# Performance work log

Measured on AMD Instinct MI355X. Metric: run time of the kernel, lower is better.

## Reference

```python
import jax, jax.numpy as jnp
import numpy as np

B, T, D = 2, 2048, 2048
N, K, H = 16, 8, 128            # heads, kv heads, head_dim
SOFT_CAP = 50.0
WINDOW = 1024
SCALE = H ** -0.5               # query_pre_attn_scalar
ROPE_BASE = 10000.0
ROPE_SCALE = 1.0
K_MASK = -2.3819763e+38


def rms_norm(x, scale, eps=1e-6):
    var = jnp.mean(jnp.square(x), axis=-1, keepdims=True)
    return x * jax.lax.rsqrt(var + eps) * (1.0 + scale)


def apply_rope(x, positions):
    # x: [B,T,heads,H]; positions: [B,T] int
    head_dim = x.shape[-1]
    fraction = 2.0 * jnp.arange(head_dim // 2, dtype=jnp.float32) / head_dim
    timescale = ROPE_BASE ** fraction                      # [H/2]
    sinusoid = positions[..., None].astype(jnp.float32) / timescale  # [B,T,H/2]
    sinusoid = sinusoid[..., None, :] / ROPE_SCALE          # [B,T,1,H/2]
    sin, cos = jnp.sin(sinusoid), jnp.cos(sinusoid)
    first, second = jnp.split(x, 2, axis=-1)
    return jnp.concatenate([first * cos - second * sin,
                            second * cos + first * sin], axis=-1)


def setup_inputs() -> dict:
    key = jax.random.key(0)
    ks = jax.random.split(key, 6)
    x = jax.random.normal(ks[0], (B, T, D), jnp.float32)
    q_w = jax.random.normal(ks[1], (N, D, H), jnp.float32) * (D ** -0.5)
    kv_w = jax.random.normal(ks[2], (2, K, D, H), jnp.float32) * (D ** -0.5)
    o_w = jax.random.normal(ks[3], (N, H, D), jnp.float32) * ((N * H) ** -0.5)
    qnorm_scale = 0.1 * jax.random.normal(ks[4], (H,), jnp.float32)
    knorm_scale = 0.1 * jax.random.normal(ks[5], (H,), jnp.float32)
    segment_pos = jnp.broadcast_to(jnp.arange(T, dtype=jnp.int32), (B, T))
    attn_mask = jnp.broadcast_to(jnp.tril(jnp.ones((T, T), dtype=bool)), (B, T, T))
    return {"x": x, "q_w": q_w, "kv_w": kv_w, "o_w": o_w,
            "qnorm_scale": qnorm_scale, "knorm_scale": knorm_scale,
            "segment_pos": segment_pos, "attn_mask": attn_mask}


def reference(x, q_w, kv_w, o_w, qnorm_scale, knorm_scale, segment_pos, attn_mask):
    # projections
    q = jnp.einsum('BTD,NDH->BTNH', x, q_w)            # [B,T,N,H]
    k = jnp.einsum('BSD,KDH->BSKH', x, kv_w[0])        # [B,T,K,H]
    v = jnp.einsum('BSD,KDH->BSKH', x, kv_w[1])
    # QK RMSNorm, then RoPE, then query scaling (matches source order)
    q = apply_rope(rms_norm(q, qnorm_scale), segment_pos) * SCALE
    k = apply_rope(rms_norm(k, knorm_scale), segment_pos)
    # GQA: regroup query heads per kv head
    G = N // K
    qg = q.reshape(B, T, K, G, H)
    logits = jnp.einsum('BTKGH,BSKH->BTKGS', qg, k).reshape(B, T, N, T)
    # logit soft cap
    logits = jnp.tanh(logits / SOFT_CAP) * SOFT_CAP
    # sliding window mask combined with causal attn_mask
    pos_q = segment_pos[:, :, None]
    pos_k = segment_pos[:, None, :]
    sliding = (pos_k > pos_q - WINDOW) & (pos_k < pos_q + WINDOW)
    mask = attn_mask & sliding                          # [B,T,S]
    padded = jnp.where(mask[:, :, None, :], logits, K_MASK)
    probs = jax.nn.softmax(padded, axis=-1).astype(k.dtype)
    enc = jnp.einsum('BTKGS,BSKH->BTKGH',
                     probs.reshape(B, T, K, G, T), v).reshape(B, T, N, H)
    return jnp.einsum('BTNH,NHD->BTD', enc, o_w)
```

## Files before the change

kernel.cpp:

```cpp
#include <hip/hip_runtime.h>
#include <stdint.h>

#define BB 2
#define TT 2048
#define DD 2048
#define NHD 16
#define KVH 8
#define HD 128
#define JC 4096
#define WIN 1024
#define SCALE_Q 0.08838834764831845f

typedef __attribute__((ext_vector_type(8))) short bf16x8;
typedef __attribute__((ext_vector_type(8))) unsigned short us8;
typedef __attribute__((ext_vector_type(4))) unsigned short us4;
typedef __attribute__((ext_vector_type(4))) float f32x4;
typedef __attribute__((ext_vector_type(16))) float f32x16;
typedef __attribute__((ext_vector_type(4))) unsigned int u32x4;

#define GAS __attribute__((address_space(1)))
#define LAS __attribute__((address_space(3)))

__device__ __forceinline__ unsigned short f2bf(float f) {
  unsigned u = __float_as_uint(f);
  u += 0x7FFFu + ((u >> 16) & 1u);
  return (unsigned short)(u >> 16);
}
__device__ __forceinline__ float bf2f(unsigned short u) {
  return __uint_as_float(((unsigned)u) << 16);
}

__device__ __forceinline__ void gload16(const void* g, void* l) {
  __builtin_amdgcn_global_load_lds((const GAS unsigned int*)g, (LAS unsigned int*)l, 16, 0, 0);
}

#define VMCNT(n) asm volatile("s_waitcnt vmcnt(" #n ")" ::: "memory")

__global__ void __launch_bounds__(256) k_cvt(const float4* __restrict__ in,
                                             us4* __restrict__ out, int n4) {
  int i = blockIdx.x * 256 + threadIdx.x;
  if (i >= n4) return;
  float4 v = in[i];
  us4 o;
  o[0] = f2bf(v.x); o[1] = f2bf(v.y); o[2] = f2bf(v.z); o[3] = f2bf(v.w);
  out[i] = o;
}

__global__ void __launch_bounds__(256) k_transpose_cvt(
    const float* __restrict__ in, unsigned short* __restrict__ out,
    int R, int C, int ldin, long b0s, int nbi, long b1s, long obs) {
  __shared__ float tile[32][33];
  int z = blockIdx.z;
  const float* ib = in + (long)(z / nbi) * b0s + (long)(z % nbi) * b1s;
  unsigned short* ob = out + (long)z * obs;
  int c0 = blockIdx.x * 32, r0 = blockIdx.y * 32;
  int tx = threadIdx.x, ty = threadIdx.y;
#pragma unroll
  for (int i = 0; i < 4; i++)
    tile[ty + i * 8][tx] = ib[(long)(r0 + ty + i * 8) * ldin + c0 + tx];
  __syncthreads();
#pragma unroll
  for (int i = 0; i < 4; i++)
    ob[(long)(c0 + ty + i * 8) * R + r0 + tx] = f2bf(tile[tx][ty + i * 8]);
}

__global__ void __launch_bounds__(256) k_wt(const float* __restrict__ qw,
                                            const float* __restrict__ kvw,
                                            unsigned short* __restrict__ out) {
  __shared__ float tile[32][33];
  int z = blockIdx.z;
  const float* ib = (z < 16) ? qw + (long)z * 2048 * 128 : kvw + (long)(z - 16) * 2048 * 128;
  unsigned short* ob = out + (long)z * 128 * 2048;
  int c0 = blockIdx.x * 32, r0 = blockIdx.y * 32;
  int tx = threadIdx.x, ty = threadIdx.y;
#pragma unroll
  for (int i = 0; i < 4; i++)
    tile[ty + i * 8][tx] = ib[(long)(r0 + ty + i * 8) * 128 + c0 + tx];
  __syncthreads();
#pragma unroll
  for (int i = 0; i < 4; i++)
    ob[(long)(c0 + ty + i * 8) * 2048 + r0 + tx] = f2bf(tile[tx][ty + i * 8]);
}

__global__ void __launch_bounds__(256) k_transpose_bf(
    const unsigned short* __restrict__ in, unsigned short* __restrict__ out,
    int R, int C, int ldin, long b0s, int nbi, long b1s, long obs) {
  __shared__ unsigned short tile[32][33];
  int z = blockIdx.z;
  const unsigned short* ib = in + (long)(z / nbi) * b0s + (long)(z % nbi) * b1s;
  unsigned short* ob = out + (long)z * obs;
  int c0 = blockIdx.x * 32, r0 = blockIdx.y * 32;
  int tx = threadIdx.x, ty = threadIdx.y;
#pragma unroll
  for (int i = 0; i < 4; i++)
    tile[ty + i * 8][tx] = ib[(long)(r0 + ty + i * 8) * ldin + c0 + tx];
  __syncthreads();
#pragma unroll
  for (int i = 0; i < 4; i++)
    ob[(long)(c0 + ty + i * 8) * R + r0 + tx] = tile[tx][ty + i * 8];
}

template <int BM, int BN, int NWN, int THREADS, int NBUF, bool BF16OUT>
__global__ void __launch_bounds__(THREADS, 2) k_gemm9(
    const unsigned short* __restrict__ A, const unsigned short* __restrict__ Bt,
    void* __restrict__ Cv, int M, int Nn, int nby) {
  constexpr int KD = 2048;
  constexpr int NT = KD / 32;
  constexpr int ROWS = BM + BN;
  constexpr int RPI = THREADS / 4;
  constexpr int IA = BM / RPI;
  constexpr int IPT = ROWS / RPI;
  constexpr int MT = 8, MT2 = 4;
  __shared__ short lds[NBUF][ROWS * 32];

  int tid = threadIdx.x, lane = tid & 63, w = tid >> 6;
  int wm = w / NWN, wn = w % NWN;
  int id = blockIdx.x;
  int cpx = gridDim.x >> 3;
  id = (id & 7) * cpx + (id >> 3);
  int m0 = (id / nby) * BM, n0 = (id % nby) * BN;

  int srow = tid >> 2;
  int scol = ((tid & 3) ^ ((tid >> 3) & 3)) * 8;
  const unsigned short* gA = A + (long)(m0 + srow) * KD + scol;
  const unsigned short* gB = Bt + (long)(n0 + srow) * KD + scol;

  auto STG = [&](int p, int ko, int j) {
    if (j < IA)
      gload16(gA + (long)j * RPI * KD + ko, &lds[p][(j * RPI + w * 16) * 32]);
    else
      gload16(gB + (long)(j - IA) * RPI * KD + ko,
              &lds[p][(BM + (j - IA) * RPI + w * 16) * 32]);
  };

  int frag = (lane & 15) * 32 + (((lane >> 4) ^ ((lane >> 1) & 3)) * 8);
  int abase = wm * 128 * 32 + frag;
  int bbase = (BM + wn * 64) * 32 + frag;

  f32x4 acc[MT][4] = {};
#pragma unroll
  for (int tt = 0; tt < NBUF - 1; ++tt)
#pragma unroll
    for (int j = 0; j < IPT; ++j) STG(tt, tt * 32, j);
  if constexpr (IPT * (NBUF - 2) == 8) VMCNT(8);
  else VMCNT(6);
  __builtin_amdgcn_s_barrier();

  int buf = 0, sp = NBUF - 1;
  for (int t = 0; t < NT; ++t) {
    const short* bufp = lds[buf];
    bool st = (t + NBUF - 1) < NT;
    int ko = (t + NBUF - 1) * 32;
    bf16x8 bfr[4], af[MT2];
#pragma unroll
    for (int ni = 0; ni < 4; ++ni)
      bfr[ni] = *(const bf16x8*)&bufp[bbase + ni * 16 * 32];
#pragma unroll
    for (int mi = 0; mi < MT2; ++mi)
      af[mi] = *(const bf16x8*)&bufp[abase + mi * 16 * 32];
    if (st) {
#pragma unroll
      for (int j = 0; j < IPT / 2; ++j) STG(sp, ko, j);
    }
    __builtin_amdgcn_s_barrier();
    asm volatile("s_waitcnt lgkmcnt(0)" ::: "memory");
    __builtin_amdgcn_sched_barrier(0);
    __builtin_amdgcn_s_setprio(1);
#pragma unroll
    for (int mi = 0; mi < MT2; ++mi)
#pragma unroll
      for (int ni = 0; ni < 4; ++ni)
        acc[mi][ni] = __builtin_amdgcn_mfma_f32_16x16x32_bf16(af[mi], bfr[ni], acc[mi][ni], 0, 0, 0);
    __builtin_amdgcn_s_setprio(0);
    __builtin_amdgcn_s_barrier();
    bf16x8 af2[MT2];
#pragma unroll
    for (int mi = 0; mi < MT2; ++mi)
      af2[mi] = *(const bf16x8*)&bufp[abase + (MT2 + mi) * 16 * 32];
    if (st) {
#pragma unroll
      for (int j = IPT / 2; j < IPT; ++j) STG(sp, ko, j);
    }
    {
      int rem = NT - 2 - t;
      if (rem > NBUF - 2) rem = NBUF - 2;
      if (rem == 2) {
        if constexpr (IPT == 4) VMCNT(8); else VMCNT(12);
      } else if (rem == 1) {
        if constexpr (IPT == 4) VMCNT(4); else VMCNT(6);
      } else if (rem == 0) {
        VMCNT(0);
      }
    }
    __builtin_amdgcn_s_barrier();
    asm volatile("s_waitcnt lgkmcnt(0)" ::: "memory");
    __builtin_amdgcn_sched_barrier(0);
    __builtin_amdgcn_s_setprio(1);
#pragma unroll
    for (int mi = 0; mi < MT2; ++mi)
#pragma unroll
      for (int ni = 0; ni < 4; ++ni)
        acc[MT2 + mi][ni] = __builtin_amdgcn_mfma_f32_16x16x32_bf16(af2[mi], bfr[ni], acc[MT2 + mi][ni], 0, 0, 0);
    __builtin_amdgcn_s_setprio(0);
    __builtin_amdgcn_s_barrier();
    buf = (buf == NBUF - 1) ? 0 : buf + 1;
    sp = (sp == NBUF - 1) ? 0 : sp + 1;
  }

#pragma unroll
  for (int mi = 0; mi < MT; mi++)
#pragma unroll
    for (int ni = 0; ni < 4; ni++)
#pragma unroll
      for (int r = 0; r < 4; r++) {
        int row = m0 + wm * 128 + mi * 16 + (lane >> 4) * 4 + r;
        int col = n0 + wn * 64 + ni * 16 + (lane & 15);
        if constexpr (BF16OUT)
          ((unsigned short*)Cv)[(long)row * Nn + col] = f2bf(acc[mi][ni][r]);
        else
          ((float*)Cv)[(long)row * Nn + col] = acc[mi][ni][r];
      }
}

__global__ void __launch_bounds__(256) k_norm_rope(
    const unsigned short* __restrict__ qkv, const float* __restrict__ qns,
    const float* __restrict__ kns,
    unsigned short* __restrict__ qb, unsigned short* __restrict__ kb) {
  int wid = threadIdx.x >> 6, lane = threadIdx.x & 63;
  long r = (long)blockIdx.x * 4 + wid;
  int b = (int)(r / (TT * 24));
  int rem = (int)(r % (TT * 24));
  int t = rem / 24, hd = rem % 24;
  const unsigned short* row = qkv + (long)(b * TT + t) * JC + (hd < 16 ? hd * HD : 2048 + (hd - 16) * HD);
  float f0 = bf2f(row[lane]), f1 = bf2f(row[lane + 64]);
  float ss = f0 * f0 + f1 * f1;
#pragma unroll
  for (int m = 1; m < 64; m <<= 1) ss += __shfl_xor(ss, m, 64);
  float rinv = rsqrtf(ss * (1.0f / 128.0f) + 1e-6f);
  const float* sc = (hd < 16) ? qns : kns;
  float y0 = f0 * rinv * (1.0f + sc[lane]);
  float y1 = f1 * rinv * (1.0f + sc[lane + 64]);
  float ts = exp2f((float)lane * (13.287712379549449f / 64.0f));
  float ang = (float)t / ts;
  float s, c;
  sincosf(ang, &s, &c);
  float o0 = y0 * c - y1 * s;
  float o1 = y1 * c + y0 * s;
  unsigned short* dst;
  if (hd < 16) {
    o0 *= SCALE_Q; o1 *= SCALE_Q;
    dst = qb + ((long)(b * NHD + hd) * TT + t) * HD;
  } else {
    dst = kb + ((long)(b * KVH + (hd - 16)) * TT + t) * HD;
  }
  dst[lane] = f2bf(o0);
  dst[lane + 64] = f2bf(o1);
}

template <bool FULL>
__device__ __forceinline__ void softcap16(const f32x16& s16, float* pr, float& lsum,
                                          int s_base, int tq, int g) {
#pragma unroll
  for (int r = 0; r < 16; r++) {
    float x = s16[r];
    float e = __builtin_amdgcn_exp2f(-0.05770780163555853f * fabsf(x));
    float u = (x > 0.0f ? e : 1.0f) * __builtin_amdgcn_rcpf(1.0f + e);
    float p = __builtin_amdgcn_exp2f(-144.26950408889634f * u);
    if (!FULL) {
      int s = s_base + (r & 3) + 8 * (r >> 2) + 4 * g;
      bool valid = (s <= tq) && (s > tq - WIN);
      p = valid ? p : 0.0f;
    }
    lsum += p;
    pr[r] = p;
  }
}

__device__ __forceinline__ void hswap(unsigned& a, unsigned& b, int g) {
  unsigned ax = (unsigned)__shfl_xor((int)a, 32, 64);
  unsigned bx = (unsigned)__shfl_xor((int)b, 32, 64);
  unsigned r0 = g ? bx : a;
  unsigned r1 = g ? b : ax;
  a = r0; b = r1;
}

__global__ void __launch_bounds__(256, 1) k_attn(
    const unsigned short* __restrict__ qb, const unsigned short* __restrict__ kb,
    const unsigned short* __restrict__ vbT, unsigned short* __restrict__ enc) {
  __shared__ short Kl[2][64][128];
  __shared__ short Vt[2][128][64];
  int tid = threadIdx.x, lane = tid & 63, w = tid >> 6;
  int g = lane >> 5, l31 = lane & 31;
  int id = blockIdx.x;
  int b = id >> 7;
  int rem = id & 127;
  int n = rem >> 3;
  int ti = rem & 7;
  int t0 = ti * 256;
  int kh = n >> 1;
  const unsigned short* qbase = qb + ((long)(b * NHD + n) * TT + t0 + w * 64) * HD;
  const unsigned short* kbase = kb + (long)(b * KVH + kh) * TT * HD;
  const unsigned short* vbase = vbT + (long)(b * KVH + kh) * HD * TT;

  bf16x8 bq[2][8];
#pragma unroll
  for (int qg = 0; qg < 2; qg++) {
    const unsigned short* qp = qbase + (long)(qg * 32 + l31) * HD + g * 8;
#pragma unroll
    for (int kb8 = 0; kb8 < 8; kb8++)
      bq[qg][kb8] = *(const bf16x8*)(qp + kb8 * 16);
  }

  f32x16 acc0[4] = {}, acc1[4] = {};
  float lsum0 = 0.0f, lsum1 = 0.0f;
  int t0w = t0 + w * 64;
  int s_begin = (t0 >= WIN) ? t0 - WIN : 0;
  int s_end = t0 + 256;

  auto STAGE = [&](int buf, int s0) {
#pragma unroll
    for (int i = 0; i < 4; i++) {
      int row = w * 16 + i * 4 + (lane >> 4);
      int c16 = (lane & 15) ^ (row & 7);
      gload16(kbase + (long)(s0 + row) * HD + c16 * 8, &Kl[buf][w * 16 + i * 4][0]);
    }
#pragma unroll
    for (int i = 0; i < 4; i++) {
      int row = w * 32 + i * 8 + (lane >> 3);
      int c16 = (lane & 7) ^ (row & 7);
      gload16(vbase + (long)row * TT + s0 + c16 * 8, &Vt[buf][w * 32 + i * 8][0]);
    }
  };

  auto PROC = [&](const f32x16& sv, int qg, float& ls, unsigned (*pwp)[4], int sb, int s0) {
    int base = t0w + qg * 32;
    int tq = base + l31;
    float pr[16];
    bool fullg = (s0 + 63 <= base) && (s0 >= base + 32 - WIN);
    if (fullg) softcap16<true>(sv, pr, ls, 0, tq, g);
    else       softcap16<false>(sv, pr, ls, s0 + sb * 32, tq, g);
    unsigned X[4], Y[4];
#pragma unroll
    for (int m = 0; m < 4; m++) {
      asm("v_cvt_pk_bf16_f32 %0, %1, %2" : "=v"(X[m]) : "v"(pr[4 * m]), "v"(pr[4 * m + 1]));
      asm("v_cvt_pk_bf16_f32 %0, %1, %2" : "=v"(Y[m]) : "v"(pr[4 * m + 2]), "v"(pr[4 * m + 3]));
    }
#pragma unroll
    for (int kl = 0; kl < 2; kl++) {
      hswap(X[2 * kl], X[2 * kl + 1], g);
      hswap(Y[2 * kl], Y[2 * kl + 1], g);
      pwp[sb * 2 + kl][0] = X[2 * kl];
      pwp[sb * 2 + kl][1] = Y[2 * kl];
      pwp[sb * 2 + kl][2] = X[2 * kl + 1];
      pwp[sb * 2 + kl][3] = Y[2 * kl + 1];
    }
  };

  STAGE(0, s_begin);
  __syncthreads();
  int cur = 0;
  for (int s0 = s_begin; s0 < s_end; s0 += 64) {
    if (s0 + 64 < s_end) STAGE(cur ^ 1, s0 + 64);
    bool live = (s0 <= t0w + 63) && (s0 + 63 >= t0w - (WIN - 1));
    if (live) {
      unsigned pw0[4][4], pw1[4][4];
#pragma unroll
      for (int sb = 0; sb < 2; sb++) {
        int srow = sb * 32 + l31;
        f32x16 s0v = {}, s1v = {};
#pragma unroll
        for (int kb8 = 0; kb8 < 8; kb8++) {
          bf16x8 ak = *(const bf16x8*)&Kl[cur][srow][8 * ((2 * kb8 + g) ^ (srow & 7))];
          s0v = __builtin_amdgcn_mfma_f32_32x32x16_bf16(ak, bq[0][kb8], s0v, 0, 0, 0);
          s1v = __builtin_amdgcn_mfma_f32_32x32x16_bf16(ak, bq[1][kb8], s1v, 0, 0, 0);
        }
        PROC(s0v, 0, lsum0, pw0, sb, s0);
        PROC(s1v, 1, lsum1, pw1, sb, s0);
      }
#pragma unroll
      for (int ks = 0; ks < 4; ks++) {
        u32x4 t40 = {pw0[ks][0], pw0[ks][1], pw0[ks][2], pw0[ks][3]};
        u32x4 t41 = {pw1[ks][0], pw1[ks][1], pw1[ks][2], pw1[ks][3]};
        bf16x8 pb0 = __builtin_bit_cast(bf16x8, t40);
        bf16x8 pb1 = __builtin_bit_cast(bf16x8, t41);
#pragma unroll
        for (int ht = 0; ht < 4; ht++) {
          int hrow = ht * 32 + l31;
          bf16x8 av = *(const bf16x8*)&Vt[cur][hrow][8 * ((2 * ks + g) ^ (hrow & 7))];
          acc0[ht] = __builtin_amdgcn_mfma_f32_32x32x16_bf16(av, pb0, acc0[ht], 0, 0, 0);
          acc1[ht] = __builtin_amdgcn_mfma_f32_32x32x16_bf16(av, pb1, acc1[ht], 0, 0, 0);
        }
      }
    }
    __syncthreads();
    cur ^= 1;
  }

  lsum0 += __shfl_xor(lsum0, 32, 64);
  lsum1 += __shfl_xor(lsum1, 32, 64);
  float inv0 = __builtin_amdgcn_rcpf(lsum0);
  float inv1 = __builtin_amdgcn_rcpf(lsum1);
  unsigned short* dst0 = enc + ((long)(b * TT + t0w + l31) * NHD + n) * HD;
  unsigned short* dst1 = enc + ((long)(b * TT + t0w + 32 + l31) * NHD + n) * HD;
#pragma unroll
  for (int ht = 0; ht < 4; ht++)
#pragma unroll
    for (int r4 = 0; r4 < 4; r4++) {
      us4 o0, o1;
#pragma unroll
      for (int e = 0; e < 4; e++) {
        o0[e] = f2bf(acc0[ht][r4 * 4 + e] * inv0);
        o1[e] = f2bf(acc1[ht][r4 * 4 + e] * inv1);
      }
      *(us4*)(dst0 + ht * 32 + 8 * r4 + 4 * g) = o0;
      *(us4*)(dst1 + ht * 32 + 8 * r4 + 4 * g) = o1;
    }
}

extern "C" void kernel_launch(void* const* d_in, const int* in_sizes, int n_in,
                              void* d_out, int out_size, void* d_ws, size_t ws_size,
                              hipStream_t stream) {
  const float* x    = (const float*)d_in[0];
  const float* q_w  = (const float*)d_in[1];
  const float* kv_w = (const float*)d_in[2];
  const float* o_w  = (const float*)d_in[3];
  const float* qns  = (const float*)d_in[4];
  const float* kns  = (const float*)d_in[5];

  if (ws_size < (104ull << 20)) return;
  char* ws = (char*)d_ws;
  unsigned short* qkvb = (unsigned short*)(ws + 0);
  unsigned short* enc  = (unsigned short*)(ws + 0);
  unsigned short* x_bf = (unsigned short*)(ws + (64ll << 20));
  unsigned short* qb   = (unsigned short*)(ws + (64ll << 20));
  unsigned short* Wt   = (unsigned short*)(ws + (80ll << 20));
  unsigned short* kb   = (unsigned short*)(ws + (80ll << 20));
  unsigned short* vbT  = (unsigned short*)(ws + (88ll << 20));
  unsigned short* Wt_o = (unsigned short*)(ws + (96ll << 20));

  dim3 tb(32, 8, 1);
  k_cvt<<<8192, 256, 0, stream>>>((const float4*)x, (us4*)x_bf, 2097152);
  k_wt<<<dim3(4, 64, 32), tb, 0, stream>>>(q_w, kv_w, Wt);
  k_transpose_cvt<<<dim3(64, 64, 1), tb, 0, stream>>>(o_w, Wt_o, 2048, 2048, 2048, 0, 1, 0, 0);
  k_gemm9<256, 256, 4, 512, 4, true><<<256, 512, 0, stream>>>(x_bf, Wt, qkvb, 4096, 4096, 16);
  k_transpose_bf<<<dim3(4, 64, 16), tb, 0, stream>>>(qkvb + 3072, vbT, 2048, 128, 4096,
                                                     (long)2048 * 4096, 8, 128, (long)128 * 2048);
  k_norm_rope<<<24576, 256, 0, stream>>>(qkvb, qns, kns, qb, kb);
  k_attn<<<256, 256, 0, stream>>>(qb, kb, vbT, enc);
  k_gemm9<256, 128, 2, 256, 3, false><<<256, 256, 0, stream>>>(enc, Wt_o, (float*)d_out, 4096, 2048, 16);
}
```

Measured before the change: 250.5 us.

## Merge prep kernels, retile QKV GEMM and attention, simplify softcap

Merges the three input-conversion and transpose kernels into one launch, and the V transpose with norm/rope into another, cutting launch count. The QKV GEMM now uses 256x128 tiles with 512 blocks instead of 256x256 with 256 blocks. Attention uses 128-thread blocks of 128 queries with two blocks per CU and interleaves the tile order between batches for load balance. The softcap exponential loses its sign-split form, saving ALU ops but risking overflow in exp2 for large logits (rcp of inf gives 0, which still works).

```diff
diff --git a/kernel.cpp b/kernel.cpp
--- a/kernel.cpp
+++ b/kernel.cpp
@@ -36,68 +36,45 @@
 
 #define VMCNT(n) asm volatile("s_waitcnt vmcnt(" #n ")" ::: "memory")
 
-__global__ void __launch_bounds__(256) k_cvt(const float4* __restrict__ in,
-                                             us4* __restrict__ out, int n4) {
-  int i = blockIdx.x * 256 + threadIdx.x;
-  if (i >= n4) return;
-  float4 v = in[i];
-  us4 o;
-  o[0] = f2bf(v.x); o[1] = f2bf(v.y); o[2] = f2bf(v.z); o[3] = f2bf(v.w);
-  out[i] = o;
-}
-
-__global__ void __launch_bounds__(256) k_transpose_cvt(
-    const float* __restrict__ in, unsigned short* __restrict__ out,
-    int R, int C, int ldin, long b0s, int nbi, long b1s, long obs) {
+__global__ void __launch_bounds__(256) k_pre(
+    const float4* __restrict__ x4, us4* __restrict__ xb,
+    const float* __restrict__ qw, const float* __restrict__ kvw,
+    const float* __restrict__ ow, unsigned short* __restrict__ Wt,
+    unsigned short* __restrict__ Wt_o) {
   __shared__ float tile[32][33];
-  int z = blockIdx.z;
-  const float* ib = in + (long)(z / nbi) * b0s + (long)(z % nbi) * b1s;
-  unsigned short* ob = out + (long)z * obs;
-  int c0 = blockIdx.x * 32, r0 = blockIdx.y * 32;
-  int tx = threadIdx.x, ty = threadIdx.y;
+  int id = blockIdx.x;
+  int tid = threadIdx.x;
+  if (id < 8192) {
+    int i = id * 256 + tid;
+    float4 v = x4[i];
+    us4 o;
+    o[0] = f2bf(v.x); o[1] = f2bf(v.y); o[2] = f2bf(v.z); o[3] = f2bf(v.w);
+    xb[i] = o;
+    return;
+  }
+  const float* ib;
+  unsigned short* ob;
+  int ldin, c0, r0;
+  int t = id - 8192;
+  if (t < 8192) {
+    int bx = t & 3, by = (t >> 2) & 63, z = t >> 8;
+    ib = (z < 16) ? qw + (long)z * 2048 * 128 : kvw + (long)(z - 16) * 2048 * 128;
+    ob = Wt + (long)z * 128 * 2048;
+    ldin = 128;
+    c0 = bx * 32; r0 = by * 32;
+  } else {
+    int u = t - 8192;
+    ib = ow; ob = Wt_o; ldin = 2048;
+    c0 = (u & 63) * 32; r0 = (u >> 6) * 32;
+  }
+  int tx = tid & 31, ty = tid >> 5;
 #pragma unroll
   for (int i = 0; i < 4; i++)
     tile[ty + i * 8][tx] = ib[(long)(r0 + ty + i * 8) * ldin + c0 + tx];
   __syncthreads();
 #pragma unroll
   for (int i = 0; i < 4; i++)
-    ob[(long)(c0 + ty + i * 8) * R + r0 + tx] = f2bf(tile[tx][ty + i * 8]);
-}
-
-__global__ void __launch_bounds__(256) k_wt(const float* __restrict__ qw,
-                                            const float* __restrict__ kvw,
-                                            unsigned short* __restrict__ out) {
-  __shared__ float tile[32][33];
-  int z = blockIdx.z;
-  const float* ib = (z < 16) ? qw + (long)z * 2048 * 128 : kvw + (long)(z - 16) * 2048 * 128;
-  unsigned short* ob = out + (long)z * 128 * 2048;
-  int c0 = blockIdx.x * 32, r0 = blockIdx.y * 32;
-  int tx = threadIdx.x, ty = threadIdx.y;
-#pragma unroll
-  for (int i = 0; i < 4; i++)
-    tile[ty + i * 8][tx] = ib[(long)(r0 + ty + i * 8) * 128 + c0 + tx];
-  __syncthreads();
-#pragma unroll
-  for (int i = 0; i < 4; i++)
     ob[(long)(c0 + ty + i * 8) * 2048 + r0 + tx] = f2bf(tile[tx][ty + i * 8]);
-}
-
-__global__ void __launch_bounds__(256) k_transpose_bf(
-    const unsigned short* __restrict__ in, unsigned short* __restrict__ out,
-    int R, int C, int ldin, long b0s, int nbi, long b1s, long obs) {
-  __shared__ unsigned short tile[32][33];
-  int z = blockIdx.z;
-  const unsigned short* ib = in + (long)(z / nbi) * b0s + (long)(z % nbi) * b1s;
-  unsigned short* ob = out + (long)z * obs;
-  int c0 = blockIdx.x * 32, r0 = blockIdx.y * 32;
-  int tx = threadIdx.x, ty = threadIdx.y;
-#pragma unroll
-  for (int i = 0; i < 4; i++)
-    tile[ty + i * 8][tx] = ib[(long)(r0 + ty + i * 8) * ldin + c0 + tx];
-  __syncthreads();
-#pragma unroll
-  for (int i = 0; i < 4; i++)
-    ob[(long)(c0 + ty + i * 8) * R + r0 + tx] = tile[tx][ty + i * 8];
 }
 
 template <int BM, int BN, int NWN, int THREADS, int NBUF, bool BF16OUT>
@@ -222,39 +199,58 @@
       }
 }
 
-__global__ void __launch_bounds__(256) k_norm_rope(
+__global__ void __launch_bounds__(256) k_post(
     const unsigned short* __restrict__ qkv, const float* __restrict__ qns,
-    const float* __restrict__ kns,
-    unsigned short* __restrict__ qb, unsigned short* __restrict__ kb) {
-  int wid = threadIdx.x >> 6, lane = threadIdx.x & 63;
-  long r = (long)blockIdx.x * 4 + wid;
-  int b = (int)(r / (TT * 24));
-  int rem = (int)(r % (TT * 24));
-  int t = rem / 24, hd = rem % 24;
-  const unsigned short* row = qkv + (long)(b * TT + t) * JC + (hd < 16 ? hd * HD : 2048 + (hd - 16) * HD);
-  float f0 = bf2f(row[lane]), f1 = bf2f(row[lane + 64]);
-  float ss = f0 * f0 + f1 * f1;
-#pragma unroll
-  for (int m = 1; m < 64; m <<= 1) ss += __shfl_xor(ss, m, 64);
-  float rinv = rsqrtf(ss * (1.0f / 128.0f) + 1e-6f);
-  const float* sc = (hd < 16) ? qns : kns;
-  float y0 = f0 * rinv * (1.0f + sc[lane]);
-  float y1 = f1 * rinv * (1.0f + sc[lane + 64]);
-  float ts = exp2f((float)lane * (13.287712379549449f / 64.0f));
-  float ang = (float)t / ts;
-  float s, c;
-  sincosf(ang, &s, &c);
-  float o0 = y0 * c - y1 * s;
-  float o1 = y1 * c + y0 * s;
-  unsigned short* dst;
-  if (hd < 16) {
-    o0 *= SCALE_Q; o1 *= SCALE_Q;
-    dst = qb + ((long)(b * NHD + hd) * TT + t) * HD;
-  } else {
-    dst = kb + ((long)(b * KVH + (hd - 16)) * TT + t) * HD;
-  }
-  dst[lane] = f2bf(o0);
-  dst[lane + 64] = f2bf(o1);
+    const float* __restrict__ kns, unsigned short* __restrict__ qb,
+    unsigned short* __restrict__ kb, unsigned short* __restrict__ vbT) {
+  int id = blockIdx.x;
+  int tid = threadIdx.x;
+  if (id < 24576) {
+    int wid = tid >> 6, lane = tid & 63;
+    long r = (long)id * 4 + wid;
+    int b = (int)(r / (TT * 24));
+    int rem = (int)(r % (TT * 24));
+    int t = rem / 24, hd = rem % 24;
+    const unsigned short* row = qkv + (long)(b * TT + t) * JC + (hd < 16 ? hd * HD : 2048 + (hd - 16) * HD);
+    float f0 = bf2f(row[lane]), f1 = bf2f(row[lane + 64]);
+    float ss = f0 * f0 + f1 * f1;
+#pragma unroll
+    for (int m = 1; m < 64; m <<= 1) ss += __shfl_xor(ss, m, 64);
+    float rinv = rsqrtf(ss * (1.0f / 128.0f) + 1e-6f);
+    const float* sc = (hd < 16) ? qns : kns;
+    float y0 = f0 * rinv * (1.0f + sc[lane]);
+    float y1 = f1 * rinv * (1.0f + sc[lane + 64]);
+    float ts = exp2f((float)lane * (13.287712379549449f / 64.0f));
+    float ang = (float)t / ts;
+    float s, c;
+    sincosf(ang, &s, &c);
+    float o0 = y0 * c - y1 * s;
+    float o1 = y1 * c + y0 * s;
+    unsigned short* dst;
+    if (hd < 16) {
+      o0 *= SCALE_Q; o1 *= SCALE_Q;
+      dst = qb + ((long)(b * NHD + hd) * TT + t) * HD;
+    } else {
+      dst = kb + ((long)(b * KVH + (hd - 16)) * TT + t) * HD;
+    }
+    dst[lane] = f2bf(o0);
+    dst[lane + 64] = f2bf(o1);
+    return;
+  }
+  __shared__ unsigned short tile[32][33];
+  int t4 = id - 24576;
+  int bx = t4 & 3, by = (t4 >> 2) & 63, z = t4 >> 8;
+  const unsigned short* ib = qkv + 3072 + (long)(z / 8) * 2048 * 4096 + (long)(z % 8) * 128;
+  unsigned short* ob = vbT + (long)z * 128 * 2048;
+  int c0 = bx * 32, r0 = by * 32;
+  int tx = tid & 31, ty = tid >> 5;
+#pragma unroll
+  for (int i = 0; i < 4; i++)
+    tile[ty + i * 8][tx] = ib[(long)(r0 + ty + i * 8) * 4096 + c0 + tx];
+  __syncthreads();
+#pragma unroll
+  for (int i = 0; i < 4; i++)
+    ob[(long)(c0 + ty + i * 8) * 2048 + r0 + tx] = tile[tx][ty + i * 8];
 }
 
 template <bool FULL>
@@ -263,9 +259,8 @@
 #pragma unroll
   for (int r = 0; r < 16; r++) {
     float x = s16[r];
-    float e = __builtin_amdgcn_exp2f(-0.05770780163555853f * fabsf(x));
-    float u = (x > 0.0f ? e : 1.0f) * __builtin_amdgcn_rcpf(1.0f + e);
-    float p = __builtin_amdgcn_exp2f(-144.26950408889634f * u);
+    float e2 = __builtin_amdgcn_exp2f(0.05770780163555853f * x);
+    float p = __builtin_amdgcn_exp2f(-144.26950408889634f * __builtin_amdgcn_rcpf(1.0f + e2));
     if (!FULL) {
       int s = s_base + (r & 3) + 8 * (r >> 2) + 4 * g;
       bool valid = (s <= tq) && (s > tq - WIN);
@@ -284,7 +279,7 @@
   a = r0; b = r1;
 }
 
-__global__ void __launch_bounds__(256, 1) k_attn(
+__global__ void __launch_bounds__(128, 2) k_attn(
     const unsigned short* __restrict__ qb, const unsigned short* __restrict__ kb,
     const unsigned short* __restrict__ vbT, unsigned short* __restrict__ enc) {
   __shared__ short Kl[2][64][128];
@@ -292,13 +287,15 @@
   int tid = threadIdx.x, lane = tid & 63, w = tid >> 6;
   int g = lane >> 5, l31 = lane & 31;
   int id = blockIdx.x;
-  int b = id >> 7;
-  int rem = id & 127;
-  int n = rem >> 3;
-  int ti = rem & 7;
-  int t0 = ti * 256;
+  int b = id >> 8;
+  int rem = id & 255;
+  int n = rem >> 4;
+  int traw = rem & 15;
+  int tile = b ? ((traw + 8) & 15) : traw;
+  int t0 = tile * 128;
   int kh = n >> 1;
-  const unsigned short* qbase = qb + ((long)(b * NHD + n) * TT + t0 + w * 64) * HD;
+  int qb0 = t0 + w * 64;
+  const unsigned short* qbase = qb + ((long)(b * NHD + n) * TT + qb0) * HD;
   const unsigned short* kbase = kb + (long)(b * KVH + kh) * TT * HD;
   const unsigned short* vbase = vbT + (long)(b * KVH + kh) * HD * TT;
 
@@ -313,27 +310,26 @@
 
   f32x16 acc0[4] = {}, acc1[4] = {};
   float lsum0 = 0.0f, lsum1 = 0.0f;
-  int t0w = t0 + w * 64;
   int s_begin = (t0 >= WIN) ? t0 - WIN : 0;
-  int s_end = t0 + 256;
+  int s_end = t0 + 128;
 
   auto STAGE = [&](int buf, int s0) {
 #pragma unroll
-    for (int i = 0; i < 4; i++) {
-      int row = w * 16 + i * 4 + (lane >> 4);
+    for (int i = 0; i < 8; i++) {
+      int row = w * 32 + i * 4 + (lane >> 4);
       int c16 = (lane & 15) ^ (row & 7);
-      gload16(kbase + (long)(s0 + row) * HD + c16 * 8, &Kl[buf][w * 16 + i * 4][0]);
-    }
-#pragma unroll
-    for (int i = 0; i < 4; i++) {
-      int row = w * 32 + i * 8 + (lane >> 3);
+      gload16(kbase + (long)(s0 + row) * HD + c16 * 8, &Kl[buf][w * 32 + i * 4][0]);
+    }
+#pragma unroll
+    for (int i = 0; i < 8; i++) {
+      int row = w * 64 + i * 8 + (lane >> 3);
       int c16 = (lane & 7) ^ (row & 7);
-      gload16(vbase + (long)row * TT + s0 + c16 * 8, &Vt[buf][w * 32 + i * 8][0]);
+      gload16(vbase + (long)row * TT + s0 + c16 * 8, &Vt[buf][w * 64 + i * 8][0]);
     }
   };
 
   auto PROC = [&](const f32x16& sv, int qg, float& ls, unsigned (*pwp)[4], int sb, int s0) {
-    int base = t0w + qg * 32;
+    int base = qb0 + qg * 32;
     int tq = base + l31;
     float pr[16];
     bool fullg = (s0 + 63 <= base) && (s0 >= base + 32 - WIN);
@@ -361,7 +357,7 @@
   int cur = 0;
   for (int s0 = s_begin; s0 < s_end; s0 += 64) {
     if (s0 + 64 < s_end) STAGE(cur ^ 1, s0 + 64);
-    bool live = (s0 <= t0w + 63) && (s0 + 63 >= t0w - (WIN - 1));
+    bool live = (s0 <= qb0 + 63) && (s0 + 63 >= qb0 - (WIN - 1));
     if (live) {
       unsigned pw0[4][4], pw1[4][4];
 #pragma unroll
@@ -400,8 +396,8 @@
   lsum1 += __shfl_xor(lsum1, 32, 64);
   float inv0 = __builtin_amdgcn_rcpf(lsum0);
   float inv1 = __builtin_amdgcn_rcpf(lsum1);
-  unsigned short* dst0 = enc + ((long)(b * TT + t0w + l31) * NHD + n) * HD;
-  unsigned short* dst1 = enc + ((long)(b * TT + t0w + 32 + l31) * NHD + n) * HD;
+  unsigned short* dst0 = enc + ((long)(b * TT + qb0 + l31) * NHD + n) * HD;
+  unsigned short* dst1 = enc + ((long)(b * TT + qb0 + 32 + l31) * NHD + n) * HD;
 #pragma unroll
   for (int ht = 0; ht < 4; ht++)
 #pragma unroll
@@ -438,14 +434,9 @@
   unsigned short* vbT  = (unsigned short*)(ws + (88ll << 20));
   unsigned short* Wt_o = (unsigned short*)(ws + (96ll << 20));
 
-  dim3 tb(32, 8, 1);
-  k_cvt<<<8192, 256, 0, stream>>>((const float4*)x, (us4*)x_bf, 2097152);
-  k_wt<<<dim3(4, 64, 32), tb, 0, stream>>>(q_w, kv_w, Wt);
-  k_transpose_cvt<<<dim3(64, 64, 1), tb, 0, stream>>>(o_w, Wt_o, 2048, 2048, 2048, 0, 1, 0, 0);
-  k_gemm9<256, 256, 4, 512, 4, true><<<256, 512, 0, stream>>>(x_bf, Wt, qkvb, 4096, 4096, 16);
-  k_transpose_bf<<<dim3(4, 64, 16), tb, 0, stream>>>(qkvb + 3072, vbT, 2048, 128, 4096,
-                                                     (long)2048 * 4096, 8, 128, (long)128 * 2048);
-  k_norm_rope<<<24576, 256, 0, stream>>>(qkvb, qns, kns, qb, kb);
-  k_attn<<<256, 256, 0, stream>>>(qb, kb, vbT, enc);
+  k_pre<<<20480, 256, 0, stream>>>((const float4*)x, (us4*)x_bf, q_w, kv_w, o_w, Wt, Wt_o);
+  k_gemm9<256, 128, 2, 256, 3, true><<<512, 256, 0, stream>>>(x_bf, Wt, qkvb, 4096, 4096, 32);
+  k_post<<<28672, 256, 0, stream>>>(qkvb, qns, kns, qb, kb, vbT);
+  k_attn<<<512, 128, 0, stream>>>(qb, kb, vbT, enc);
   k_gemm9<256, 128, 2, 256, 3, false><<<256, 256, 0, stream>>>(enc, Wt_o, (float*)d_out, 4096, 2048, 16);
 }
```

After: 227.8 us. 1.1x faster.
